# Kernel optimization log

Hardware: AMD Instinct MI355X
Metric: run time of the kernel (lower is better)

Reference implementation:

```python
import jax, jax.numpy as jnp
import numpy as np

NUM_HEADS = 1  # the module's reshape only type-checks for num_heads == 1 (see notes)


def setup_inputs() -> dict:
    key = jax.random.key(0)
    ks = jax.random.split(key, 9)
    B, S, H = 16, 4096, 512
    std = 0.02
    return {
        "x": jax.random.normal(ks[0], (B, S, H), dtype=jnp.float32),
        "Wq": jax.random.normal(ks[1], (H, H), dtype=jnp.float32) * std,
        "bq": jnp.zeros((H,), dtype=jnp.float32),
        "Wk": jax.random.normal(ks[2], (H, H), dtype=jnp.float32) * std,
        "bk": jnp.zeros((H,), dtype=jnp.float32),
        "Wv": jax.random.normal(ks[3], (H, H), dtype=jnp.float32) * std,
        "bv": jnp.zeros((H,), dtype=jnp.float32),
        "Wo": jax.random.normal(ks[4], (H, H), dtype=jnp.float32) * std,
        "bo": jnp.zeros((H,), dtype=jnp.float32),
    }


def reference(x, Wq, bq, Wk, bk, Wv, bv, Wo, bo):
    B, S, H = x.shape
    nh = NUM_HEADS
    hd = H // nh
    # Faithful to the torch code: view(B*nh, S, hd).transpose(1, 2) -> (G, hd, S)
    q = (x @ Wq + bq).reshape(B * nh, S, hd).transpose(0, 2, 1)  # (G, hd, S)
    k = (x @ Wk + bk).reshape(B * nh, S, hd).transpose(0, 2, 1)  # (G, hd, S)
    v = (x @ Wv + bv).reshape(B * nh, S, hd).transpose(0, 2, 1)  # (G, hd, S)
    # Attention matrix is over feature dims: (G, hd, hd), contraction over S
    scores = jnp.einsum('gds,ges->gde', q, k) / jnp.sqrt(jnp.float32(hd))
    attn = jax.nn.softmax(scores, axis=-1)                        # (G, hd, hd)
    attn_out = jnp.einsum('gde,ges->gds', attn, v)                # (G, hd, S)
    attn_out = attn_out.transpose(0, 2, 1)                        # (G, S, hd) == (B, S, H) for nh=1
    return attn_out @ Wo + bo
```

## Files before the change

### kernel.cpp

```cpp
#include <hip/hip_runtime.h>
#include <hip/hip_bf16.h>


typedef __attribute__((ext_vector_type(4))) float f32x4;
typedef __attribute__((ext_vector_type(8))) __bf16 bf16x8;
typedef __attribute__((ext_vector_type(4))) __bf16 bf16x4;

typedef __attribute__((address_space(1))) const void gconst_void;
typedef __attribute__((address_space(3))) void lds_void;

__device__ __forceinline__ void gload_lds16(const void* g, void* l) {
  __builtin_amdgcn_global_load_lds((gconst_void*)g, (lds_void*)l, 16, 0, 0);
}

__device__ __forceinline__ void cvt_hilo(float v, __bf16& h, __bf16& l) {
  h = (__bf16)v;
  l = (__bf16)(v - (float)h);
}

template <int MODE>
__global__ __launch_bounds__(256) void gemm3p(
    const void* Ap, const void* ApLo,
    const void* Bp, const void* BpLo,
    float* __restrict__ C,
    int M, int N, int K,
    long long sAg, long long sBg, long long sCg,
    const float* bias, long long sBiasG,
    float alpha)
{
  constexpr int LD = (MODE == 1) ? 64 : 72;
  __shared__ __align__(16) __bf16 sAhi[128 * LD];
  __shared__ __align__(16) __bf16 sAlo[128 * LD];
  __shared__ __align__(16) __bf16 sBhi[128 * LD];
  __shared__ __align__(16) __bf16 sBlo[128 * LD];

  const int t = threadIdx.x;
  const int g = blockIdx.z;
  const int m0 = blockIdx.y * 128, n0 = blockIdx.x * 128;
  const int lane = t & 63;
  const int w = t >> 6, wm = w >> 1, wn = w & 1;
  const int lr = lane & 15, lg = lane >> 4;

  const f32x4 fzero = {0.f, 0.f, 0.f, 0.f};
  f32x4 acc[4][4];
#pragma unroll
  for (int i = 0; i < 4; ++i)
#pragma unroll
    for (int j = 0; j < 4; ++j) acc[i][j] = fzero;

  for (int k0 = 0; k0 < K; k0 += 64) {
    __syncthreads();
    if constexpr (MODE == 1) {
      const __bf16* Ah = (const __bf16*)Ap + g * sAg;
      const __bf16* Al = (const __bf16*)ApLo + g * sAg;
      const __bf16* Bh = (const __bf16*)Bp + g * sBg;
      const __bf16* Bl = (const __bf16*)BpLo + g * sBg;
#pragma unroll
      for (int it = 0; it < 4; ++it) {
        int r = it * 32 + (t >> 3);
        int sl = (t & 7) ^ (r & 7);
        long long ea = (long long)(m0 + r) * K + k0 + sl * 8;
        long long eb = (long long)(n0 + r) * K + k0 + sl * 8;
        int dst = it * 4096 + (t >> 6) * 1024;
        gload_lds16(Ah + ea, (char*)sAhi + dst);
        gload_lds16(Al + ea, (char*)sAlo + dst);
        gload_lds16(Bh + eb, (char*)sBhi + dst);
        gload_lds16(Bl + eb, (char*)sBlo + dst);
      }
    } else {
      const float* A = (const float*)Ap + g * sAg;
      const float* B = (const float*)Bp + g * sBg;
      const int f = t & 15, r0 = t >> 4;
#pragma unroll
      for (int p = 0; p < 8; ++p) {
        int r = r0 + p * 16;
        float4 va = *(const float4*)(A + (long long)(m0 + r) * K + k0 + f * 4);
        float4 vb = *(const float4*)(B + (long long)(n0 + r) * K + k0 + f * 4);
        bf16x4 ah4, al4, bh4, bl4;
        __bf16 hh, ll;
        cvt_hilo(va.x, hh, ll); ah4[0] = hh; al4[0] = ll;
        cvt_hilo(va.y, hh, ll); ah4[1] = hh; al4[1] = ll;
        cvt_hilo(va.z, hh, ll); ah4[2] = hh; al4[2] = ll;
        cvt_hilo(va.w, hh, ll); ah4[3] = hh; al4[3] = ll;
        cvt_hilo(vb.x, hh, ll); bh4[0] = hh; bl4[0] = ll;
        cvt_hilo(vb.y, hh, ll); bh4[1] = hh; bl4[1] = ll;
        cvt_hilo(vb.z, hh, ll); bh4[2] = hh; bl4[2] = ll;
        cvt_hilo(vb.w, hh, ll); bh4[3] = hh; bl4[3] = ll;
        *(bf16x4*)&sAhi[r * LD + f * 4] = ah4;
        *(bf16x4*)&sAlo[r * LD + f * 4] = al4;
        *(bf16x4*)&sBhi[r * LD + f * 4] = bh4;
        *(bf16x4*)&sBlo[r * LD + f * 4] = bl4;
      }
    }
    __syncthreads();
#pragma unroll
    for (int ks = 0; ks < 2; ++ks) {
      bf16x8 ah[4], al[4], bh[4], bl[4];
#pragma unroll
      for (int i = 0; i < 4; ++i) {
        int ra = wm * 64 + i * 16 + lr;
        int rb = wn * 64 + i * 16 + lr;
        int oa, ob;
        if constexpr (MODE == 1) {
          oa = ra * 64 + (((ks * 4 + lg) ^ (ra & 7)) * 8);
          ob = rb * 64 + (((ks * 4 + lg) ^ (rb & 7)) * 8);
        } else {
          oa = ra * LD + ks * 32 + lg * 8;
          ob = rb * LD + ks * 32 + lg * 8;
        }
        ah[i] = *(const bf16x8*)&sAhi[oa];
        al[i] = *(const bf16x8*)&sAlo[oa];
        bh[i] = *(const bf16x8*)&sBhi[ob];
        bl[i] = *(const bf16x8*)&sBlo[ob];
      }
#pragma unroll
      for (int i = 0; i < 4; ++i)
#pragma unroll
        for (int j = 0; j < 4; ++j) {
          acc[i][j] = __builtin_amdgcn_mfma_f32_16x16x32_bf16(ah[i], bh[j], acc[i][j], 0, 0, 0);
          acc[i][j] = __builtin_amdgcn_mfma_f32_16x16x32_bf16(ah[i], bl[j], acc[i][j], 0, 0, 0);
          acc[i][j] = __builtin_amdgcn_mfma_f32_16x16x32_bf16(al[i], bh[j], acc[i][j], 0, 0, 0);
        }
    }
  }

  float* Cg = C + g * sCg;
  const float* bg = bias ? bias + g * sBiasG : nullptr;
#pragma unroll
  for (int i = 0; i < 4; ++i) {
    int row = m0 + wm * 64 + i * 16 + lg * 4;
#pragma unroll
    for (int j = 0; j < 4; ++j) {
      int col = n0 + wn * 64 + j * 16 + lr;
      float bb = bg ? bg[col] : 0.0f;
#pragma unroll
      for (int q = 0; q < 4; ++q)
        Cg[(long long)(row + q) * N + col] = acc[i][j][q] * alpha + bb;
    }
  }
}

__global__ __launch_bounds__(256) void transcvt_k(
    const float* __restrict__ x, __bf16* __restrict__ xTh, __bf16* __restrict__ xTl)
{
  __shared__ float tile[64][65];
  const int g = blockIdx.z, h0 = blockIdx.x * 64, s0 = blockIdx.y * 64;
  const int t = threadIdx.x, f = t & 15, r0 = t >> 4;
#pragma unroll
  for (int p = 0; p < 4; ++p) {
    int r = r0 + p * 16;
    float4 v = *(const float4*)(x + ((long long)g * 4096 + s0 + r) * 512 + h0 + f * 4);
    tile[f * 4 + 0][r] = v.x;
    tile[f * 4 + 1][r] = v.y;
    tile[f * 4 + 2][r] = v.z;
    tile[f * 4 + 3][r] = v.w;
  }
  __syncthreads();
  const int hr = t >> 2, sc = t & 3;
  long long ob = ((long long)g * 512 + h0 + hr) * 4096 + s0 + sc * 16;
#pragma unroll
  for (int i4 = 0; i4 < 4; ++i4) {
    bf16x4 hv, lv;
#pragma unroll
    for (int q = 0; q < 4; ++q) {
      __bf16 hh, ll;
      cvt_hilo(tile[hr][sc * 16 + i4 * 4 + q], hh, ll);
      hv[q] = hh; lv[q] = ll;
    }
    *(bf16x4*)(xTh + ob + i4 * 4) = hv;
    *(bf16x4*)(xTl + ob + i4 * 4) = lv;
  }
}

__global__ __launch_bounds__(256) void transp_k(
    const float* __restrict__ src, float* __restrict__ dst,
    int M, int N, long long sg, long long sgT)
{
  __shared__ float tile[64][65];
  const int g = blockIdx.z, n0 = blockIdx.x * 64, m0 = blockIdx.y * 64;
  const int t = threadIdx.x, f = t & 15, r0 = t >> 4;
  const float* s = src + g * sg;
  float* d = dst + g * sgT;
#pragma unroll
  for (int p = 0; p < 4; ++p) {
    int r = r0 + p * 16;
    float4 v = *(const float4*)(s + (long long)(m0 + r) * N + n0 + f * 4);
    tile[f * 4 + 0][r] = v.x;
    tile[f * 4 + 1][r] = v.y;
    tile[f * 4 + 2][r] = v.z;
    tile[f * 4 + 3][r] = v.w;
  }
  __syncthreads();
  const int nr = t >> 2, mc = t & 3;
#pragma unroll
  for (int i4 = 0; i4 < 4; ++i4) {
    float4 o;
    o.x = tile[nr][mc * 16 + i4 * 4 + 0];
    o.y = tile[nr][mc * 16 + i4 * 4 + 1];
    o.z = tile[nr][mc * 16 + i4 * 4 + 2];
    o.w = tile[nr][mc * 16 + i4 * 4 + 3];
    *(float4*)(d + (long long)(n0 + nr) * M + m0 + mc * 16 + i4 * 4) = o;
  }
}

__global__ __launch_bounds__(256) void colsum_k(const float* __restrict__ x, float* __restrict__ ssum)
{
  const int g = blockIdx.z, h = blockIdx.x * 256 + threadIdx.x, sb = blockIdx.y;
  float p = 0.f;
  for (int s = sb * 64; s < sb * 64 + 64; ++s)
    p += x[((long long)g * 4096 + s) * 512 + h];
  atomicAdd(&ssum[g * 512 + h], p);
}

__global__ __launch_bounds__(256) void rk_k(
    const float* __restrict__ ssum, const float* __restrict__ Wq, const float* __restrict__ Wk,
    float* __restrict__ rho, float* __restrict__ kap)
{
  const int g = blockIdx.y, d = blockIdx.x * 256 + threadIdx.x;
  float r = 0.f, k = 0.f;
  for (int f = 0; f < 512; ++f) {
    float s = ssum[g * 512 + f];
    r += s * Wq[f * 512 + d];
    k += s * Wk[f * 512 + d];
  }
  rho[g * 512 + d] = r;
  kap[g * 512 + d] = k;
}

__global__ __launch_bounds__(256) void softmax_k(
    float* __restrict__ SC, const float* __restrict__ rho, const float* __restrict__ kap,
    const float* __restrict__ bq, const float* __restrict__ bk, float alpha)
{
  const int rowid = blockIdx.x * 4 + (threadIdx.x >> 6);
  const int g = rowid >> 9, d = rowid & 511;
  const int l = threadIdx.x & 63;
  float* row = SC + (long long)rowid * 512;
  const float bqd = bq[d];
  const float rr = rho[g * 512 + d] + 4096.f * bqd;
  float4 z0 = *(float4*)(row + l * 8);
  float4 z1 = *(float4*)(row + l * 8 + 4);
  float4 bk0 = *(const float4*)(bk + l * 8);
  float4 bk1 = *(const float4*)(bk + l * 8 + 4);
  float4 kp0 = *(const float4*)(kap + g * 512 + l * 8);
  float4 kp1 = *(const float4*)(kap + g * 512 + l * 8 + 4);
  float z[8];
  z[0] = z0.x + alpha * (bqd * kp0.x + bk0.x * rr);
  z[1] = z0.y + alpha * (bqd * kp0.y + bk0.y * rr);
  z[2] = z0.z + alpha * (bqd * kp0.z + bk0.z * rr);
  z[3] = z0.w + alpha * (bqd * kp0.w + bk0.w * rr);
  z[4] = z1.x + alpha * (bqd * kp1.x + bk1.x * rr);
  z[5] = z1.y + alpha * (bqd * kp1.y + bk1.y * rr);
  z[6] = z1.z + alpha * (bqd * kp1.z + bk1.z * rr);
  z[7] = z1.w + alpha * (bqd * kp1.w + bk1.w * rr);
  float m = z[0];
#pragma unroll
  for (int j = 1; j < 8; ++j) m = fmaxf(m, z[j]);
  for (int o = 32; o; o >>= 1) m = fmaxf(m, __shfl_xor(m, o));
  float sum = 0.f;
#pragma unroll
  for (int j = 0; j < 8; ++j) { z[j] = __expf(z[j] - m); sum += z[j]; }
  for (int o = 32; o; o >>= 1) sum += __shfl_xor(sum, o);
  const float inv = 1.0f / sum;
  *(float4*)(row + l * 8)     = make_float4(z[0] * inv, z[1] * inv, z[2] * inv, z[3] * inv);
  *(float4*)(row + l * 8 + 4) = make_float4(z[4] * inv, z[5] * inv, z[6] * inv, z[7] * inv);
}

__global__ __launch_bounds__(256) void cvec_k(
    const float* __restrict__ Aat, const float* __restrict__ bv, const float* __restrict__ bo,
    float* __restrict__ c)
{
  const int g = blockIdx.z, h = blockIdx.x * 256 + threadIdx.x, eb = blockIdx.y;
  float p = (eb == 0) ? bo[h] : 0.f;
  for (int e = eb * 64; e < eb * 64 + 64; ++e)
    p += bv[e] * Aat[((long long)g * 512 + e) * 512 + h];
  atomicAdd(&c[g * 512 + h], p);
}

extern "C" void kernel_launch(void* const* d_in, const int* in_sizes, int n_in,
                              void* d_out, int out_size, void* d_ws, size_t ws_size,
                              hipStream_t stream) {
  (void)in_sizes; (void)n_in; (void)out_size; (void)ws_size;
  const float* x  = (const float*)d_in[0];
  const float* Wq = (const float*)d_in[1];
  const float* bq = (const float*)d_in[2];
  const float* Wk = (const float*)d_in[3];
  const float* bk = (const float*)d_in[4];
  const float* Wv = (const float*)d_in[5];
  const float* bv = (const float*)d_in[6];
  const float* Wo = (const float*)d_in[7];
  const float* bo = (const float*)d_in[8];
  float* out = (float*)d_out;

  char* ws = (char*)d_ws;
  __bf16* xTh = (__bf16*)(ws);
  __bf16* xTl = (__bf16*)(ws + 67108864);
  float* S1   = (float*)(ws + 134217728);
  float* S2   = (float*)(ws + 150994944);
  float* S3   = (float*)(ws + 167772160);
  float* WqT  = (float*)(ws + 184549376);
  float* WkT  = (float*)(ws + 185597952);
  float* WoT  = (float*)(ws + 186646528);
  float* ssum = (float*)(ws + 187695104);
  float* cbuf = (float*)(ws + 187695104 + 32768);
  float* rho  = (float*)(ws + 187695104 + 65536);
  float* kap  = (float*)(ws + 187695104 + 98304);

  const long long SXT = 512LL * 4096;
  const long long SM  = 512LL * 512;
  const long long SX  = 4096LL * 512;
  const float alpha = 0.04419417382415922f;

  hipMemsetAsync(ssum, 0, 65536, stream);

  colsum_k<<<dim3(2, 64, 16), 256, 0, stream>>>(x, ssum);
  transcvt_k<<<dim3(8, 64, 16), 256, 0, stream>>>(x, xTh, xTl);
  rk_k<<<dim3(2, 16), 256, 0, stream>>>(ssum, Wq, Wk, rho, kap);
  transp_k<<<dim3(8, 8, 1), 256, 0, stream>>>(Wq, WqT, 512, 512, 0, 0);
  transp_k<<<dim3(8, 8, 1), 256, 0, stream>>>(Wk, WkT, 512, 512, 0, 0);
  transp_k<<<dim3(8, 8, 1), 256, 0, stream>>>(Wo, WoT, 512, 512, 0, 0);

  gemm3p<1><<<dim3(4, 4, 16), 256, 0, stream>>>(
      xTh, xTl, xTh, xTl, S1, 512, 512, 4096, SXT, SXT, SM, nullptr, 0, 1.0f);
  gemm3p<0><<<dim3(4, 4, 16), 256, 0, stream>>>(
      WkT, nullptr, S1, nullptr, S2, 512, 512, 512, 0, SM, SM, nullptr, 0, 1.0f);
  gemm3p<0><<<dim3(4, 4, 16), 256, 0, stream>>>(
      WqT, nullptr, S2, nullptr, S3, 512, 512, 512, 0, SM, SM, nullptr, 0, alpha);
  softmax_k<<<2048, 256, 0, stream>>>(S3, rho, kap, bq, bk, alpha);
  transp_k<<<dim3(8, 8, 16), 256, 0, stream>>>(S3, S1, 512, 512, SM, SM);
  gemm3p<0><<<dim3(4, 4, 16), 256, 0, stream>>>(
      S1, nullptr, WoT, nullptr, S2, 512, 512, 512, SM, 0, SM, nullptr, 0, 1.0f);
  cvec_k<<<dim3(2, 8, 16), 256, 0, stream>>>(S2, bv, bo, cbuf);
  transp_k<<<dim3(8, 8, 16), 256, 0, stream>>>(S2, S3, 512, 512, SM, SM);
  gemm3p<0><<<dim3(4, 4, 16), 256, 0, stream>>>(
      S3, nullptr, Wv, nullptr, S1, 512, 512, 512, SM, 0, SM, nullptr, 0, 1.0f);
  gemm3p<0><<<dim3(4, 32, 16), 256, 0, stream>>>(
      x, nullptr, S1, nullptr, out, 4096, 512, 512, SX, SM, SX, cbuf, 512, 1.0f);
}
```

Before: 855.8 us.

## Exploit Gram symmetry, split-K, smaller tiles, and prequantized operands for final GEMM

The x^T x Gram GEMM now computes only lower-triangle tiles with split-K, accumulating through atomics into a zeroed buffer, then mirrors the result with a triangle-only transpose. The column sum is fused into the transpose-convert kernel, and the three weight transposes are merged into one launch. The small 512x512 GEMMs use 64-wide tiles to launch more blocks. The final large GEMM now uses pre-split bf16 hi/lo operands loaded straight into LDS instead of converting in the inner loop. The costs are extra conversion passes over x, atomic contention, and in-place transpose hazards.

```diff
diff --git a/kernel.cpp b/kernel.cpp
--- a/kernel.cpp
+++ b/kernel.cpp
@@ -18,7 +18,7 @@
   l = (__bf16)(v - (float)h);
 }
 
-template <int MODE>
+template <int MODE, int BMN>
 __global__ __launch_bounds__(256) void gemm3p(
     const void* Ap, const void* ApLo,
     const void* Bp, const void* BpLo,
@@ -26,29 +26,41 @@
     int M, int N, int K,
     long long sAg, long long sBg, long long sCg,
     const float* bias, long long sBiasG,
-    float alpha)
+    float alpha, int tri, int splitK)
 {
   constexpr int LD = (MODE == 1) ? 64 : 72;
-  __shared__ __align__(16) __bf16 sAhi[128 * LD];
-  __shared__ __align__(16) __bf16 sAlo[128 * LD];
-  __shared__ __align__(16) __bf16 sBhi[128 * LD];
-  __shared__ __align__(16) __bf16 sBlo[128 * LD];
+  constexpr int R = BMN / 32;
+  __shared__ __align__(16) __bf16 sAhi[BMN * LD];
+  __shared__ __align__(16) __bf16 sAlo[BMN * LD];
+  __shared__ __align__(16) __bf16 sBhi[BMN * LD];
+  __shared__ __align__(16) __bf16 sBlo[BMN * LD];
 
   const int t = threadIdx.x;
   const int g = blockIdx.z;
-  const int m0 = blockIdx.y * 128, n0 = blockIdx.x * 128;
+  int m0, n0, kBeg, kEnd;
+  if (tri) {
+    int p = blockIdx.x, bx = 0;
+    while ((bx + 1) * (bx + 2) / 2 <= p) ++bx;
+    int by = p - bx * (bx + 1) / 2;
+    m0 = bx * BMN; n0 = by * BMN;
+    int kLen = K / splitK;
+    kBeg = blockIdx.y * kLen; kEnd = kBeg + kLen;
+  } else {
+    m0 = blockIdx.y * BMN; n0 = blockIdx.x * BMN;
+    kBeg = 0; kEnd = K;
+  }
   const int lane = t & 63;
   const int w = t >> 6, wm = w >> 1, wn = w & 1;
   const int lr = lane & 15, lg = lane >> 4;
 
   const f32x4 fzero = {0.f, 0.f, 0.f, 0.f};
-  f32x4 acc[4][4];
-#pragma unroll
-  for (int i = 0; i < 4; ++i)
-#pragma unroll
-    for (int j = 0; j < 4; ++j) acc[i][j] = fzero;
-
-  for (int k0 = 0; k0 < K; k0 += 64) {
+  f32x4 acc[R][R];
+#pragma unroll
+  for (int i = 0; i < R; ++i)
+#pragma unroll
+    for (int j = 0; j < R; ++j) acc[i][j] = fzero;
+
+  for (int k0 = kBeg; k0 < kEnd; k0 += 64) {
     __syncthreads();
     if constexpr (MODE == 1) {
       const __bf16* Ah = (const __bf16*)Ap + g * sAg;
@@ -56,7 +68,7 @@
       const __bf16* Bh = (const __bf16*)Bp + g * sBg;
       const __bf16* Bl = (const __bf16*)BpLo + g * sBg;
 #pragma unroll
-      for (int it = 0; it < 4; ++it) {
+      for (int it = 0; it < BMN / 32; ++it) {
         int r = it * 32 + (t >> 3);
         int sl = (t & 7) ^ (r & 7);
         long long ea = (long long)(m0 + r) * K + k0 + sl * 8;
@@ -72,7 +84,7 @@
       const float* B = (const float*)Bp + g * sBg;
       const int f = t & 15, r0 = t >> 4;
 #pragma unroll
-      for (int p = 0; p < 8; ++p) {
+      for (int p = 0; p < BMN / 16; ++p) {
         int r = r0 + p * 16;
         float4 va = *(const float4*)(A + (long long)(m0 + r) * K + k0 + f * 4);
         float4 vb = *(const float4*)(B + (long long)(n0 + r) * K + k0 + f * 4);
@@ -95,11 +107,11 @@
     __syncthreads();
 #pragma unroll
     for (int ks = 0; ks < 2; ++ks) {
-      bf16x8 ah[4], al[4], bh[4], bl[4];
-#pragma unroll
-      for (int i = 0; i < 4; ++i) {
-        int ra = wm * 64 + i * 16 + lr;
-        int rb = wn * 64 + i * 16 + lr;
+      bf16x8 ah[R], al[R], bh[R], bl[R];
+#pragma unroll
+      for (int i = 0; i < R; ++i) {
+        int ra = wm * (BMN / 2) + i * 16 + lr;
+        int rb = wn * (BMN / 2) + i * 16 + lr;
         int oa, ob;
         if constexpr (MODE == 1) {
           oa = ra * 64 + (((ks * 4 + lg) ^ (ra & 7)) * 8);
@@ -114,9 +126,9 @@
         bl[i] = *(const bf16x8*)&sBlo[ob];
       }
 #pragma unroll
-      for (int i = 0; i < 4; ++i)
-#pragma unroll
-        for (int j = 0; j < 4; ++j) {
+      for (int i = 0; i < R; ++i)
+#pragma unroll
+        for (int j = 0; j < R; ++j) {
           acc[i][j] = __builtin_amdgcn_mfma_f32_16x16x32_bf16(ah[i], bh[j], acc[i][j], 0, 0, 0);
           acc[i][j] = __builtin_amdgcn_mfma_f32_16x16x32_bf16(ah[i], bl[j], acc[i][j], 0, 0, 0);
           acc[i][j] = __builtin_amdgcn_mfma_f32_16x16x32_bf16(al[i], bh[j], acc[i][j], 0, 0, 0);
@@ -127,21 +139,28 @@
   float* Cg = C + g * sCg;
   const float* bg = bias ? bias + g * sBiasG : nullptr;
 #pragma unroll
-  for (int i = 0; i < 4; ++i) {
-    int row = m0 + wm * 64 + i * 16 + lg * 4;
-#pragma unroll
-    for (int j = 0; j < 4; ++j) {
-      int col = n0 + wn * 64 + j * 16 + lr;
-      float bb = bg ? bg[col] : 0.0f;
-#pragma unroll
-      for (int q = 0; q < 4; ++q)
-        Cg[(long long)(row + q) * N + col] = acc[i][j][q] * alpha + bb;
+  for (int i = 0; i < R; ++i) {
+    int row = m0 + wm * (BMN / 2) + i * 16 + lg * 4;
+#pragma unroll
+    for (int j = 0; j < R; ++j) {
+      int col = n0 + wn * (BMN / 2) + j * 16 + lr;
+      if (splitK > 1) {
+#pragma unroll
+        for (int q = 0; q < 4; ++q)
+          atomicAdd(&Cg[(long long)(row + q) * N + col], acc[i][j][q] * alpha);
+      } else {
+        float bb = bg ? bg[col] : 0.0f;
+#pragma unroll
+        for (int q = 0; q < 4; ++q)
+          Cg[(long long)(row + q) * N + col] = acc[i][j][q] * alpha + bb;
+      }
     }
   }
 }
 
 __global__ __launch_bounds__(256) void transcvt_k(
-    const float* __restrict__ x, __bf16* __restrict__ xTh, __bf16* __restrict__ xTl)
+    const float* __restrict__ x, __bf16* __restrict__ xTh, __bf16* __restrict__ xTl,
+    float* __restrict__ ssum)
 {
   __shared__ float tile[64][65];
   const int g = blockIdx.z, h0 = blockIdx.x * 64, s0 = blockIdx.y * 64;
@@ -158,26 +177,33 @@
   __syncthreads();
   const int hr = t >> 2, sc = t & 3;
   long long ob = ((long long)g * 512 + h0 + hr) * 4096 + s0 + sc * 16;
+  float csum = 0.f;
 #pragma unroll
   for (int i4 = 0; i4 < 4; ++i4) {
     bf16x4 hv, lv;
 #pragma unroll
     for (int q = 0; q < 4; ++q) {
+      float vv = tile[hr][sc * 16 + i4 * 4 + q];
+      csum += vv;
       __bf16 hh, ll;
-      cvt_hilo(tile[hr][sc * 16 + i4 * 4 + q], hh, ll);
+      cvt_hilo(vv, hh, ll);
       hv[q] = hh; lv[q] = ll;
     }
     *(bf16x4*)(xTh + ob + i4 * 4) = hv;
     *(bf16x4*)(xTl + ob + i4 * 4) = lv;
   }
+  csum += __shfl_xor(csum, 1);
+  csum += __shfl_xor(csum, 2);
+  if ((t & 3) == 0) atomicAdd(&ssum[g * 512 + h0 + hr], csum);
 }
 
 __global__ __launch_bounds__(256) void transp_k(
     const float* __restrict__ src, float* __restrict__ dst,
-    int M, int N, long long sg, long long sgT)
+    int M, int N, long long sg, long long sgT, int triOnly)
 {
   __shared__ float tile[64][65];
   const int g = blockIdx.z, n0 = blockIdx.x * 64, m0 = blockIdx.y * 64;
+  if (triOnly && m0 <= n0) return;
   const int t = threadIdx.x, f = t & 15, r0 = t >> 4;
   const float* s = src + g * sg;
   float* d = dst + g * sgT;
@@ -203,13 +229,54 @@
   }
 }
 
-__global__ __launch_bounds__(256) void colsum_k(const float* __restrict__ x, float* __restrict__ ssum)
-{
-  const int g = blockIdx.z, h = blockIdx.x * 256 + threadIdx.x, sb = blockIdx.y;
-  float p = 0.f;
-  for (int s = sb * 64; s < sb * 64 + 64; ++s)
-    p += x[((long long)g * 4096 + s) * 512 + h];
-  atomicAdd(&ssum[g * 512 + h], p);
+__global__ __launch_bounds__(256) void wtrans_k(
+    const float* __restrict__ Wq, const float* __restrict__ Wk, const float* __restrict__ Wo,
+    float* __restrict__ WqT, float* __restrict__ WkT, float* __restrict__ WoT)
+{
+  __shared__ float tile[64][65];
+  const int z = blockIdx.z;
+  const float* s = (z == 0) ? Wq : (z == 1) ? Wk : Wo;
+  float* d = (z == 0) ? WqT : (z == 1) ? WkT : WoT;
+  const int n0 = blockIdx.x * 64, m0 = blockIdx.y * 64;
+  const int t = threadIdx.x, f = t & 15, r0 = t >> 4;
+#pragma unroll
+  for (int p = 0; p < 4; ++p) {
+    int r = r0 + p * 16;
+    float4 v = *(const float4*)(s + (long long)(m0 + r) * 512 + n0 + f * 4);
+    tile[f * 4 + 0][r] = v.x;
+    tile[f * 4 + 1][r] = v.y;
+    tile[f * 4 + 2][r] = v.z;
+    tile[f * 4 + 3][r] = v.w;
+  }
+  __syncthreads();
+  const int nr = t >> 2, mc = t & 3;
+#pragma unroll
+  for (int i4 = 0; i4 < 4; ++i4) {
+    float4 o;
+    o.x = tile[nr][mc * 16 + i4 * 4 + 0];
+    o.y = tile[nr][mc * 16 + i4 * 4 + 1];
+    o.z = tile[nr][mc * 16 + i4 * 4 + 2];
+    o.w = tile[nr][mc * 16 + i4 * 4 + 3];
+    *(float4*)(d + (long long)(n0 + nr) * 512 + m0 + mc * 16 + i4 * 4) = o;
+  }
+}
+
+__global__ __launch_bounds__(256) void cvt32_k(
+    const float* __restrict__ src, __bf16* __restrict__ h, __bf16* __restrict__ l,
+    long long n4)
+{
+  long long stride = (long long)gridDim.x * 256;
+  for (long long i = blockIdx.x * 256LL + threadIdx.x; i < n4; i += stride) {
+    float4 v = ((const float4*)src)[i];
+    bf16x4 hv, lv;
+    __bf16 hh, ll;
+    cvt_hilo(v.x, hh, ll); hv[0] = hh; lv[0] = ll;
+    cvt_hilo(v.y, hh, ll); hv[1] = hh; lv[1] = ll;
+    cvt_hilo(v.z, hh, ll); hv[2] = hh; lv[2] = ll;
+    cvt_hilo(v.w, hh, ll); hv[3] = hh; lv[3] = ll;
+    *(bf16x4*)(h + i * 4) = hv;
+    *(bf16x4*)(l + i * 4) = lv;
+  }
 }
 
 __global__ __launch_bounds__(256) void rk_k(
@@ -305,34 +372,43 @@
   float* rho  = (float*)(ws + 187695104 + 65536);
   float* kap  = (float*)(ws + 187695104 + 98304);
 
+  __bf16* PThi = (__bf16*)S2;
+  __bf16* PTlo = (__bf16*)((char*)S2 + 8388608);
+  __bf16* xnh = xTh;
+  __bf16* xnl = xTl;
+
   const long long SXT = 512LL * 4096;
   const long long SM  = 512LL * 512;
   const long long SX  = 4096LL * 512;
   const float alpha = 0.04419417382415922f;
 
   hipMemsetAsync(ssum, 0, 65536, stream);
-
-  colsum_k<<<dim3(2, 64, 16), 256, 0, stream>>>(x, ssum);
-  transcvt_k<<<dim3(8, 64, 16), 256, 0, stream>>>(x, xTh, xTl);
+  hipMemsetAsync(S1, 0, 16777216, stream);
+
+  transcvt_k<<<dim3(8, 64, 16), 256, 0, stream>>>(x, xTh, xTl, ssum);
+  wtrans_k<<<dim3(8, 8, 3), 256, 0, stream>>>(Wq, Wk, Wo, WqT, WkT, WoT);
   rk_k<<<dim3(2, 16), 256, 0, stream>>>(ssum, Wq, Wk, rho, kap);
-  transp_k<<<dim3(8, 8, 1), 256, 0, stream>>>(Wq, WqT, 512, 512, 0, 0);
-  transp_k<<<dim3(8, 8, 1), 256, 0, stream>>>(Wk, WkT, 512, 512, 0, 0);
-  transp_k<<<dim3(8, 8, 1), 256, 0, stream>>>(Wo, WoT, 512, 512, 0, 0);
-
-  gemm3p<1><<<dim3(4, 4, 16), 256, 0, stream>>>(
-      xTh, xTl, xTh, xTl, S1, 512, 512, 4096, SXT, SXT, SM, nullptr, 0, 1.0f);
-  gemm3p<0><<<dim3(4, 4, 16), 256, 0, stream>>>(
-      WkT, nullptr, S1, nullptr, S2, 512, 512, 512, 0, SM, SM, nullptr, 0, 1.0f);
-  gemm3p<0><<<dim3(4, 4, 16), 256, 0, stream>>>(
-      WqT, nullptr, S2, nullptr, S3, 512, 512, 512, 0, SM, SM, nullptr, 0, alpha);
+
+  gemm3p<1, 128><<<dim3(10, 4, 16), 256, 0, stream>>>(
+      xTh, xTl, xTh, xTl, S1, 512, 512, 4096, SXT, SXT, SM, nullptr, 0, 1.0f, 1, 4);
+  transp_k<<<dim3(8, 8, 16), 256, 0, stream>>>(S1, S1, 512, 512, SM, SM, 1);
+
+  gemm3p<0, 64><<<dim3(8, 8, 16), 256, 0, stream>>>(
+      WkT, nullptr, S1, nullptr, S2, 512, 512, 512, 0, SM, SM, nullptr, 0, 1.0f, 0, 1);
+  gemm3p<0, 64><<<dim3(8, 8, 16), 256, 0, stream>>>(
+      WqT, nullptr, S2, nullptr, S3, 512, 512, 512, 0, SM, SM, nullptr, 0, alpha, 0, 1);
   softmax_k<<<2048, 256, 0, stream>>>(S3, rho, kap, bq, bk, alpha);
-  transp_k<<<dim3(8, 8, 16), 256, 0, stream>>>(S3, S1, 512, 512, SM, SM);
-  gemm3p<0><<<dim3(4, 4, 16), 256, 0, stream>>>(
-      S1, nullptr, WoT, nullptr, S2, 512, 512, 512, SM, 0, SM, nullptr, 0, 1.0f);
+  transp_k<<<dim3(8, 8, 16), 256, 0, stream>>>(S3, S1, 512, 512, SM, SM, 0);
+  gemm3p<0, 64><<<dim3(8, 8, 16), 256, 0, stream>>>(
+      S1, nullptr, WoT, nullptr, S2, 512, 512, 512, SM, 0, SM, nullptr, 0, 1.0f, 0, 1);
   cvec_k<<<dim3(2, 8, 16), 256, 0, stream>>>(S2, bv, bo, cbuf);
-  transp_k<<<dim3(8, 8, 16), 256, 0, stream>>>(S2, S3, 512, 512, SM, SM);
-  gemm3p<0><<<dim3(4, 4, 16), 256, 0, stream>>>(
-      S3, nullptr, Wv, nullptr, S1, 512, 512, 512, SM, 0, SM, nullptr, 0, 1.0f);
-  gemm3p<0><<<dim3(4, 32, 16), 256, 0, stream>>>(
-      x, nullptr, S1, nullptr, out, 4096, 512, 512, SX, SM, SX, cbuf, 512, 1.0f);
-}
+  transp_k<<<dim3(8, 8, 16), 256, 0, stream>>>(S2, S3, 512, 512, SM, SM, 0);
+  gemm3p<0, 64><<<dim3(8, 8, 16), 256, 0, stream>>>(
+      S3, nullptr, Wv, nullptr, S1, 512, 512, 512, SM, 0, SM, nullptr, 0, 1.0f, 0, 1);
+
+  cvt32_k<<<2048, 256, 0, stream>>>(S1, PThi, PTlo, 16LL * 512 * 512 / 4);
+  cvt32_k<<<2048, 256, 0, stream>>>(x, xnh, xnl, 16LL * 4096 * 512 / 4);
+
+  gemm3p<1, 128><<<dim3(4, 32, 16), 256, 0, stream>>>(
+      xnh, xnl, PThi, PTlo, out, 4096, 512, 512, SX, SM, SX, cbuf, 512, 1.0f, 0, 1);
+}
```

Measured after the change: 717.3 us. 1.19x faster.
